# Performance work log

Hardware: AMD Instinct MI355X
Metric: run time of the kernel (lower is better)

## Reference

```python
import jax, jax.numpy as jnp
import numpy as np
import math

NEG_INF = -1e9
B, Q, M, P, HID, H, S = 4, 512, 512, 128, 1024, 16, 64
R = M + Q            # 1024, key length
POSLEN = M + 2 * Q   # 1536


def rel_shift(x):
    # x: [N, H, Q, Rp] -> relative-shifted, same shape
    n, h, q, rp = x.shape
    padded = jnp.pad(x, ((0, 0), (0, 0), (0, 0), (1, 0)))
    return padded.reshape(n, h, rp + 1, q)[:, :, 1:].reshape(n, h, q, rp)


def _attention(query, token_mask, key_content, value, key_position,
               segment_encoding, segment_matrix,
               content_bias, position_bias, segment_bias):
    # query: [N,Q,H,S]; key_content/value: [N,R,H,S]; key_position: [N,Rp,H,S]
    r = key_content.shape[1]
    content_att = jnp.einsum('nqhs,nrhs->nhqr', query + content_bias, key_content)
    position_att = jnp.einsum('nqhs,nrhs->nhqr', query + position_bias, key_position)
    position_att = rel_shift(position_att)[..., 1:1 + r]
    segment_att = jnp.einsum('nqhs,ghs->nhqg', query + segment_bias, segment_encoding)
    # select same-segment (g=1) vs diff-segment (g=0) logit per (q, r) pair
    segment_att = jnp.where(segment_matrix[:, None],           # [N,1,Q,R]
                            segment_att[..., 1:],              # [N,H,Q,1]
                            segment_att[..., :1])
    scale = 1.0 / math.sqrt(float(S))
    logits = (content_att + position_att + segment_att) * scale
    logits = logits + token_mask * NEG_INF
    weights = jax.nn.softmax(logits, axis=3)
    return jnp.einsum('nhqr,nrhs->nqhs', weights, value)


def setup_inputs() -> dict:
    key = jax.random.key(0)
    ks = jax.random.split(key, 16)
    sc = 0.05
    content_inputs = jax.random.normal(ks[0], (B, Q, HID), jnp.float32)
    query_inputs = jax.random.normal(ks[1], (B, P, HID), jnp.float32)
    position_encoding = jax.random.normal(ks[2], (B, POSLEN, HID), jnp.float32)
    segment_encoding = jax.random.normal(ks[3], (2, H, S), jnp.float32) * sc
    segment_matrix = jax.random.randint(ks[4], (B, Q, R), 0, 2) > 0
    # one-hot target mapping: P distinct target positions per batch row
    tpos = jax.vmap(lambda k: jax.random.permutation(k, Q)[:P])(jax.random.split(ks[5], B))
    target_mapping = jax.nn.one_hot(tpos, Q, dtype=jnp.float32)  # [B,P,Q]
    # causal-style permutation masks (1 = masked)
    causal = (jnp.arange(R)[None, :] > (jnp.arange(Q)[:, None] + M)).astype(jnp.float32)
    content_mask = jnp.broadcast_to(causal[None, None], (B, 1, Q, R))
    diag = jnp.pad(jnp.eye(Q, dtype=jnp.float32), ((0, 0), (M, 0)))
    query_mask = jnp.broadcast_to(jnp.minimum(causal + diag, 1.0)[None, None], (B, 1, Q, R))
    content_bias = jax.random.normal(ks[6], (H, S), jnp.float32) * sc
    position_bias = jax.random.normal(ks[7], (H, S), jnp.float32) * sc
    segment_bias = jax.random.normal(ks[8], (H, S), jnp.float32) * sc
    mems = jax.random.normal(ks[9], (B, M, HID), jnp.float32)
    wsc = 1.0 / math.sqrt(HID)
    Wq = jax.random.normal(ks[10], (HID, H, S), jnp.float32) * wsc
    Wkc = jax.random.normal(ks[11], (HID, H, S), jnp.float32) * wsc
    Wv = jax.random.normal(ks[12], (HID, H, S), jnp.float32) * wsc
    Wkp = jax.random.normal(ks[13], (HID, H, S), jnp.float32) * wsc
    Wo = jax.random.normal(ks[14], (H, S, HID), jnp.float32) * wsc
    return dict(content_inputs=content_inputs, query_inputs=query_inputs,
                position_encoding=position_encoding, segment_encoding=segment_encoding,
                segment_matrix=segment_matrix, target_mapping=target_mapping,
                content_mask=content_mask, query_mask=query_mask,
                content_bias=content_bias, position_bias=position_bias,
                segment_bias=segment_bias, mems=mems,
                Wq=Wq, Wkc=Wkc, Wv=Wv, Wkp=Wkp, Wo=Wo)


def reference(content_inputs, query_inputs, position_encoding, segment_encoding,
              segment_matrix, target_mapping, content_mask, query_mask,
              content_bias, position_bias, segment_bias, mems,
              Wq, Wkc, Wv, Wkp, Wo):
    split = lambda x, w: jnp.einsum('nld,dhs->nlhs', x, w)
    merge = lambda x, w: jnp.einsum('nlhs,hsd->nld', x, w)
    contexts = jnp.concatenate([mems, content_inputs], axis=1)  # [B,R,HID]
    key_content = split(contexts, Wkc)
    value = split(contexts, Wv)
    key_position = split(position_encoding, Wkp)
    attn = lambda q, m: _attention(q, m, key_content, value, key_position,
                                   segment_encoding, segment_matrix,
                                   content_bias, position_bias, segment_bias)
    # content stream
    q_c = split(content_inputs, Wq)
    content_outputs = merge(attn(q_c, content_mask), Wo)
    # query stream, scattered to target positions via one-hot target_mapping
    q_q = split(query_inputs, Wq)                               # [B,P,H,S]
    q_q = jnp.einsum('nphs,npq->nqhs', q_q, target_mapping)     # [B,Q,H,S]
    query_outputs = attn(q_q, query_mask)
    query_outputs = jnp.einsum('nqhs,npq->nphs', query_outputs, target_mapping)
    query_outputs = merge(query_outputs, Wo)
    return content_outputs, query_outputs
```

## Files before the change

kernel.cpp:

```cpp
#include <hip/hip_runtime.h>
#include <hip/hip_bf16.h>
#include <math.h>

#define B_ 4
#define Q_ 512
#define M_ 512
#define P_ 128
#define HID_ 1024
#define H_ 16
#define S_ 64
#define R_ 1024
#define POSLEN_ 1536

typedef short bf16x8 __attribute__((ext_vector_type(8)));
typedef float f32x4 __attribute__((ext_vector_type(4)));
typedef unsigned int u32;
typedef unsigned long long u64;

__device__ __forceinline__ ushort f2bf(float f) {
    u32 u = __float_as_uint(f);
    u32 r = (u + 0x7fffu + ((u >> 16) & 1u)) >> 16;
    return (ushort)r;
}
__device__ __forceinline__ float bf2f(ushort s) {
    return __uint_as_float(((u32)s) << 16);
}
__device__ __forceinline__ void gload16(void* l, const void* g) {
    __builtin_amdgcn_global_load_lds(
        (const __attribute__((address_space(1))) u32*)g,
        (__attribute__((address_space(3))) u32*)l, 16, 0, 0);
}

__global__ void find_tpos_k(const float* __restrict__ tm, int* __restrict__ tpos) {
    int i = blockIdx.x * blockDim.x + threadIdx.x;
    if (i >= B_ * P_) return;
    const float* row = tm + (size_t)i * Q_;
    int q = 0;
    for (int j = 0; j < Q_; ++j) q = (row[j] > 0.5f) ? j : q;
    tpos[i] = q;
}

__global__ __launch_bounds__(256) void cvt_all(
    const float* __restrict__ content, const float* __restrict__ mems,
    const float* __restrict__ posenc,  const float* __restrict__ query,
    ushort* __restrict__ ctx, ushort* __restrict__ pos,
    ushort* __restrict__ cont, ushort* __restrict__ qry)
{
    int v = blockIdx.x * 256 + threadIdx.x;
    const float* src;
    ushort* dst;
    if (v < 524288) {
        int row = v >> 7, c8 = v & 127;
        int n = row >> 10, l = row & 1023;
        src = (l < M_) ? mems + ((size_t)(n * M_ + l)) * 1024 + c8 * 8
                       : content + ((size_t)(n * Q_ + (l - M_))) * 1024 + c8 * 8;
        dst = ctx + (size_t)v * 8;
    } else if (v < 1310720) {
        int u = v - 524288;
        src = posenc + (size_t)u * 8; dst = pos + (size_t)u * 8;
    } else if (v < 1572864) {
        int u = v - 1310720;
        src = content + (size_t)u * 8; dst = cont + (size_t)u * 8;
    } else {
        int u = v - 1572864;
        src = query + (size_t)u * 8; dst = qry + (size_t)u * 8;
    }
    float4 a = *(const float4*)src;
    float4 b = *(const float4*)(src + 4);
    ushort4 o0 = {f2bf(a.x), f2bf(a.y), f2bf(a.z), f2bf(a.w)};
    ushort4 o1 = {f2bf(b.x), f2bf(b.y), f2bf(b.z), f2bf(b.w)};
    *(ushort4*)dst = o0;
    *(ushort4*)(dst + 4) = o1;
}

__global__ __launch_bounds__(256) void transpose5(
    const float* W0, const float* W1, const float* W2, const float* W3, const float* W4,
    ushort* T0, ushort* T1, ushort* T2, ushort* T3, ushort* T4)
{
    __shared__ float t[32][33];
    const float* W; ushort* T;
    switch (blockIdx.z) {
        case 0: W = W0; T = T0; break;
        case 1: W = W1; T = T1; break;
        case 2: W = W2; T = T2; break;
        case 3: W = W3; T = T3; break;
        default: W = W4; T = T4; break;
    }
    int bx = blockIdx.x * 32, by = blockIdx.y * 32;
    int tx = threadIdx.x & 31, ty = threadIdx.x >> 5;
    #pragma unroll
    for (int i = 0; i < 32; i += 8)
        t[ty + i][tx] = W[(size_t)(by + ty + i) * 1024 + bx + tx];
    __syncthreads();
    #pragma unroll
    for (int i = 0; i < 32; i += 8)
        T[(size_t)(bx + ty + i) * 1024 + by + tx] = f2bf(t[tx][ty + i]);
}

__global__ __launch_bounds__(256) void seg_prep(const float* __restrict__ segenc,
                                                const float* __restrict__ cb,
                                                const float* __restrict__ sb,
                                                ushort* __restrict__ seg_bf,
                                                float* __restrict__ segc) {
    for (int t = threadIdx.x; t < 16 * 16 * 64; t += 256) {
        int h = t >> 10, g = (t >> 6) & 15, s = t & 63;
// ... 130 lines not shown
    #pragma unroll
    for (int i = 0; i < 4; ++i)
        #pragma unroll
        for (int j = 0; j < 2; ++j) acc[i][j] = f32x4{0.f, 0.f, 0.f, 0.f};

    for (int k0 = 0; k0 < 1024; k0 += 64) {
        __syncthreads();
        #pragma unroll
        for (int it = 0; it < 4; ++it) {
            int idx = it * 256 + tid;
            gload16(&As[idx * 8], A + (size_t)(m0 + (idx >> 3)) * 1024 + k0 + (idx & 7) * 8);
        }
        #pragma unroll
        for (int it = 0; it < 2; ++it) {
            int idx = it * 256 + tid;
            gload16(&Bs[idx * 8], Wo_t + (size_t)(n0 + (idx >> 3)) * 1024 + k0 + (idx & 7) * 8);
        }
        __syncthreads();
        #pragma unroll
        for (int kk = 0; kk < 2; ++kk) {
            const int krd = kk * 32 + hi * 8;
            bf16x8 af[4], bfr[2];
            #pragma unroll
            for (int i = 0; i < 4; ++i)
                af[i] = *(const bf16x8*)&As[(wm * 64 + i * 16 + l15) * 64 + krd];
            #pragma unroll
            for (int j = 0; j < 2; ++j)
                bfr[j] = *(const bf16x8*)&Bs[(wn * 32 + j * 16 + l15) * 64 + krd];
            #pragma unroll
            for (int i = 0; i < 4; ++i)
                #pragma unroll
                for (int j = 0; j < 2; ++j)
                    acc[i][j] = __builtin_amdgcn_mfma_f32_16x16x32_bf16(af[i], bfr[j], acc[i][j], 0, 0, 0);
        }
    }
    #pragma unroll
    for (int i = 0; i < 4; ++i)
        #pragma unroll
        for (int j = 0; j < 2; ++j) {
            int col = n0 + wn * 32 + j * 16 + l15;
            #pragma unroll
            for (int r = 0; r < 4; ++r) {
                int row = m0 + wm * 64 + i * 16 + hi * 4 + r;
                C[(size_t)row * 1024 + col] = acc[i][j][r];
            }
        }
}

__global__ __launch_bounds__(256) void pa_gemm(const ushort* __restrict__ Qpb,
                                               const ushort* __restrict__ KPb,
                                               ushort* __restrict__ PA) {
    const int tid = threadIdx.x;
    const int lane = tid & 63, w = tid >> 6;
    const int l15 = lane & 15, hi = lane >> 4;
    const int jt = blockIdx.x * 128, nh = blockIdx.y;
    const int p0 = w * 32;

    bf16x8 a[2][2];
    #pragma unroll
    for (int i = 0; i < 2; ++i)
        #pragma unroll
        for (int kk = 0; kk < 2; ++kk)
            a[i][kk] = *(const bf16x8*)(Qpb + ((size_t)(nh * 128 + p0 + i * 16 + l15)) * 64 + kk * 32 + hi * 8);

    #pragma unroll
    for (int jc = 0; jc < 8; ++jc) {
        f32x4 c0 = {0.f,0.f,0.f,0.f}, c1 = {0.f,0.f,0.f,0.f};
        #pragma unroll
        for (int kk = 0; kk < 2; ++kk) {
            bf16x8 b = *(const bf16x8*)(KPb + ((size_t)nh * 1536 + jt + jc * 16 + l15) * 64 + kk * 32 + hi * 8);
            c0 = __builtin_amdgcn_mfma_f32_16x16x32_bf16(a[0][kk], b, c0, 0, 0, 0);
            c1 = __builtin_amdgcn_mfma_f32_16x16x32_bf16(a[1][kk], b, c1, 0, 0, 0);
        }
        #pragma unroll
        for (int r = 0; r < 4; ++r) {
            PA[((size_t)(nh * 128 + p0 + hi * 4 + r)) * 1536 + jt + jc * 16 + l15] = f2bf(c0[r]);
            PA[((size_t)(nh * 128 + p0 + 16 + hi * 4 + r)) * 1536 + jt + jc * 16 + l15] = f2bf(c1[r]);
        }
    }
}

#define EXSC 0.180336879f
#define EXBI -23.0831204f
__global__ __launch_bounds__(128) void attn_uni(
    const ushort* __restrict__ Qccb, const ushort* __restrict__ Qcpb,
    const ushort* __restrict__ Qqcb,
    const ushort* __restrict__ KCb,  const ushort* __restrict__ KPb,
    const ushort* __restrict__ Vtb,  const ushort* __restrict__ segb,
    const float* __restrict__ segc,  const u64* __restrict__ pseg,
    const int* __restrict__ tpos,    const ushort* __restrict__ PA,
    float* __restrict__ Pp)
{
    __shared__ ushort Kt[2][64 * 64];
    __shared__ ushort DlT[2][96 * 34];
    __shared__ ushort Pl[2][32 * 64];

    const int tid = threadIdx.x;
    const int lane = tid & 63, wv = tid >> 6;
    const int l15 = lane & 15, hi = lane >> 4;

    int wg = blockIdx.x + 10 * (blockIdx.y + 32 * blockIdx.z);
    int swz = (wg & 7) * 160 + (wg >> 3);
    const int bx = swz % 10;
    int rem = swz / 10;
    const int gy = rem & 31;
    const int n = rem >> 5;

    const bool ISQ = bx >= 8;
    const int h = gy & 15, half = gy >> 4;
    const int nh = n * 16 + h;
    const int q0w = (ISQ ? (bx - 8) * 64 : bx * 64) + wv * 32;

    ushort* dlt = DlT[wv];
    ushort* pl  = Pl[wv];

    bf16x8 acb[2][2], apb[2][2];
    {
        const ushort* qc = ISQ ? (Qqcb + ((size_t)nh * P_ + q0w) * 64)
                               : (Qccb + ((size_t)nh * Q_ + q0w) * 64);
        #pragma unroll
        for (int i = 0; i < 2; ++i)
            #pragma unroll
            for (int kk = 0; kk < 2; ++kk)
                acb[i][kk] = *(const bf16x8*)(qc + (size_t)(i * 16 + l15) * 64 + kk * 32 + hi * 8);
        if (!ISQ) {
            const ushort* qp = Qcpb + ((size_t)nh * Q_ + q0w) * 64;
            #pragma unroll
            for (int i = 0; i < 2; ++i)
                #pragma unroll
                for (int kk = 0; kk < 2; ++kk)
                    apb[i][kk] = *(const bf16x8*)(qp + (size_t)(i * 16 + l15) * 64 + kk * 32 + hi * 8);
        } else {
            apb[0][0] = acb[0][0]; apb[0][1] = acb[0][1];
            apb[1][0] = acb[1][0]; apb[1][1] = acb[1][1];
        }
    }

    float sd[2][2][4];
    {
        f32x4 sg[2] = {{0.f,0.f,0.f,0.f},{0.f,0.f,0.f,0.f}};
        #pragma unroll
        for (int kk = 0; kk < 2; ++kk) {
            bf16x8 b = *(const bf16x8*)(segb + (size_t)(h * 16 + l15) * 64 + kk * 32 + hi * 8);
            sg[0] = __builtin_amdgcn_mfma_f32_16x16x32_bf16(acb[0][kk], b, sg[0], 0, 0, 0);
            sg[1] = __builtin_amdgcn_mfma_f32_16x16x32_bf16(acb[1][kk], b, sg[1], 0, 0, 0);
        }
        float c0 = segc[h * 2 + 0], c1 = segc[h * 2 + 1];
        #pragma unroll
        for (int i = 0; i < 2; ++i)
            #pragma unroll
            for (int r = 0; r < 4; ++r) {
                int base = (lane & 48) << 2;
                sd[0][i][r] = __int_as_float(__builtin_amdgcn_ds_bpermute(base, __float_as_int(sg[i][r]))) + c0;
                sd[1][i][r] = __int_as_float(__builtin_amdgcn_ds_bpermute(base + 4, __float_as_int(sg[i][r]))) + c1;
            }
    }

    int qg[2][4];
    #pragma unroll
    for (int i = 0; i < 2; ++i)
        #pragma unroll
        for (int r = 0; r < 4; ++r) {
            int p = q0w + i * 16 + hi * 4 + r;
            qg[i][r] = ISQ ? tpos[n * P_ + p] : p;
        }

    f32x4 acc[2][4];
    float psum[2][4] = {};
    #pragma unroll
    for (int i = 0; i < 2; ++i)
        #pragma unroll
        for (int j = 0; j < 4; ++j) acc[i][j] = f32x4{0.f,0.f,0.f,0.f};

    auto stage = [&](int b, int rt) {
        const int r0s = rt * 64;
        #pragma unroll
        for (int it = 0; it < 4; ++it) {
            int e = it * 128 + tid;
            int row = e >> 3;
            int sc = ((e & 7) * 8) ^ ((row & 7) << 3);
            gload16(&Kt[b][e * 8], KCb + ((size_t)nh * R_ + r0s + row) * 64 + sc);
        }
    };

    const int q0top = (ISQ ? (bx - 8) * 64 : bx * 64) + 32;
    const int ntb = ISQ ? 16 : min(16, ((q0top + 543) >> 6) + 1);
    const int nt1 = (ntb + 1) >> 1;
    const int t0 = half ? nt1 : 0;
    const int tmax = half ? ntb : nt1;

    stage(0, t0);
    __syncthreads();
    int buf = 0;

    for (int rt = t0; rt < tmax; ++rt) {
        const int r0 = rt * 64;
        if (rt + 1 < tmax) stage(buf ^ 1, rt + 1);

        const bool skip = !ISQ && (r0 > q0w + 543);
        if (!skip) {
            bf16x8 vf[2][4];
            #pragma unroll
            for (int kk = 0; kk < 2; ++kk)
                #pragma unroll
                for (int dj = 0; dj < 4; ++dj)
                    vf[kk][dj] = *(const bf16x8*)(Vtb + ((size_t)nh * 64 + dj * 16 + l15) * 1024 + r0 + kk * 32 + hi * 8);

            f32x4 s[2][4];
            #pragma unroll
            for (int i = 0; i < 2; ++i)
                #pragma unroll
                for (int fc = 0; fc < 4; ++fc) s[i][fc] = f32x4{0.f,0.f,0.f,0.f};
            #pragma unroll
            for (int kk = 0; kk < 2; ++kk) {
                #pragma unroll
                for (int fc = 0; fc < 4; ++fc) {
                    int krow = fc * 16 + l15;
                    bf16x8 kb = *(const bf16x8*)&Kt[buf][krow * 64 + ((kk * 32 + hi * 8) ^ ((krow & 7) << 3))];
                    s[0][fc] = __builtin_amdgcn_mfma_f32_16x16x32_bf16(acb[0][kk], kb, s[0][fc], 0, 0, 0);
                    s[1][fc] = __builtin_amdgcn_mfma_f32_16x16x32_bf16(acb[1][kk], kb, s[1][fc], 0, 0, 0);
                }
            }

            if (!ISQ) {
                const int jb0 = r0 - q0w + 481;
                #pragma unroll
                for (int t = 0; t < 6; ++t) {
                    f32x4 d0 = {0.f,0.f,0.f,0.f}, d1 = {0.f,0.f,0.f,0.f};
                    #pragma unroll
                    for (int kk = 0; kk < 2; ++kk) {
                        bf16x8 pv = *(const bf16x8*)(KPb + ((size_t)nh * POSLEN_ + jb0 + t * 16 + l15) * 64 + kk * 32 + hi * 8);
                        d0 = __builtin_amdgcn_mfma_f32_16x16x32_bf16(apb[0][kk], pv, d0, 0, 0, 0);
                        d1 = __builtin_amdgcn_mfma_f32_16x16x32_bf16(apb[1][kk], pv, d1, 0, 0, 0);
                    }
                    int jj = (t * 16 + l15) * 34;
                    *(u32*)&dlt[jj + hi * 4]          = (u32)f2bf(d0[0]) | ((u32)f2bf(d0[1]) << 16);
                    *(u32*)&dlt[jj + hi * 4 + 2]      = (u32)f2bf(d0[2]) | ((u32)f2bf(d0[3]) << 16);
                    *(u32*)&dlt[jj + 16 + hi * 4]     = (u32)f2bf(d1[0]) | ((u32)f2bf(d1[1]) << 16);
                    *(u32*)&dlt[jj + 16 + hi * 4 + 2] = (u32)f2bf(d1[2]) | ((u32)f2bf(d1[3]) << 16);
                }
            }

            float pav[2][4][4];
            if (ISQ) {
                #pragma unroll
                for (int i = 0; i < 2; ++i)
                    #pragma unroll
                    for (int fc = 0; fc < 4; ++fc)
                        #pragma unroll
                        for (int r = 0; r < 4; ++r) {
                            int qq = i * 16 + hi * 4 + r;
                            int j = (r0 + fc * 16 + l15) - qg[i][r] + 512;
                            pav[i][fc][r] = bf2f(PA[((size_t)nh * P_ + q0w + qq) * 1536 + j]);
                        }
            }

            #pragma unroll
            for (int i = 0; i < 2; ++i) {
                u64 sw[4];
                #pragma unroll
                for (int r = 0; r < 4; ++r)
                    sw[r] = pseg[((size_t)n * Q_ + qg[i][r]) * 16 + rt];
                #pragma unroll
                for (int fc = 0; fc < 4; ++fc) {
                    #pragma unroll
                    for (int r = 0; r < 4; ++r) {
                        int qq = i * 16 + hi * 4 + r;
                        int rr = fc * 16 + l15;
                        float dval = ISQ ? pav[i][fc][r] : bf2f(dlt[(rr - qq + 31) * 34 + qq]);
                        int sel = (int)((sw[r] >> rr) & 1);
                        float st = s[i][fc][r] + dval + (sel ? sd[1][i][r] : sd[0][i][r]);
                        float v = fmaf(st, EXSC, EXBI);
                        bool masked = ISQ ? ((r0 + rr) >= qg[i][r] + 512)
                                          : ((r0 + rr) > qg[i][r] + 512);
                        v = masked ? -INFINITY : v;
                        float pv = exp2f(v);
                        ushort us = f2bf(pv);
                        psum[i][r] += bf2f(us);
                        int row = i * 16 + hi * 4 + r;
                        int cc = (fc * 16 + l15) ^ ((row & 7) << 3);
                        pl[row * 64 + cc] = us;
                    }
                }
            }

            #pragma unroll
            for (int kk = 0; kk < 2; ++kk) {
                bf16x8 pa[2];
                #pragma unroll
                for (int i = 0; i < 2; ++i) {
                    int row = i * 16 + l15;
                    int cc = (kk * 32 + hi * 8) ^ ((row & 7) << 3);
                    pa[i] = *(const bf16x8*)&pl[row * 64 + cc];
                }
                #pragma unroll
                for (int dj = 0; dj < 4; ++dj) {
                    acc[0][dj] = __builtin_amdgcn_mfma_f32_16x16x32_bf16(pa[0], vf[kk][dj], acc[0][dj], 0, 0, 0);
                    acc[1][dj] = __builtin_amdgcn_mfma_f32_16x16x32_bf16(pa[1], vf[kk][dj], acc[1][dj], 0, 0, 0);
                }
            }
        }
        __syncthreads();
        buf ^= 1;
    }

    #pragma unroll
    for (int i = 0; i < 2; ++i)
        #pragma unroll
        for (int r = 0; r < 4; ++r) {
            #pragma unroll
            for (int d = 1; d < 16; d <<= 1) psum[i][r] += __shfl_xor(psum[i][r], d, 64);
        }

    #pragma unroll
    for (int i = 0; i < 2; ++i)
        #pragma unroll
        for (int r = 0; r < 4; ++r) {
            int qrow = q0w + i * 16 + hi * 4 + r;
            size_t rowg = ISQ ? (32768 + (size_t)nh * P_ + qrow) : ((size_t)nh * Q_ + qrow);
            float* base = Pp + (rowg * 2 + half) * 72;
            #pragma unroll
            for (int dj = 0; dj < 4; ++dj)
                base[dj * 16 + l15] = acc[i][dj][r];
            if (l15 == 0) base[64] = psum[i][r];
        }
}

__global__ __launch_bounds__(256) void combine_k(const float* __restrict__ Pp,
                                                 ushort* __restrict__ AOc,
                                                 ushort* __restrict__ AOq) {
    int idx = blockIdx.x * 256 + threadIdx.x;
    int row = idx >> 6, d = idx & 63;
    const float* b0 = Pp + ((size_t)row * 2 + 0) * 72;
    const float* b1 = b0 + 72;
    float l = b0[64] + b1[64];
    ushort o = f2bf((b0[d] + b1[d]) / l);
    if (row < 32768) {
        int n = row >> 13, h = (row >> 9) & 15, q = row & 511;
        AOc[((size_t)(n * Q_ + q)) * 1024 + h * 64 + d] = o;
    } else {
        int r2 = row - 32768;
        int n = r2 >> 11, h = (r2 >> 7) & 15, p = r2 & 127;
        AOq[((size_t)(n * P_ + p)) * 1024 + h * 64 + d] = o;
    }
}

extern "C" void kernel_launch(void* const* d_in, const int* in_sizes, int n_in,
                              void* d_out, int out_size, void* d_ws, size_t ws_size,
                              hipStream_t stream) {
    const float* content = (const float*)d_in[0];
    const float* query   = (const float*)d_in[1];
    const float* posenc  = (const float*)d_in[2];
    const float* segenc  = (const float*)d_in[3];
    const int*   segmat  = (const int*)d_in[4];
    const float* tmap    = (const float*)d_in[5];
    const float* cbias   = (const float*)d_in[8];
    const float* pbias   = (const float*)d_in[9];
    const float* sbias   = (const float*)d_in[10];
    const float* mems    = (const float*)d_in[11];
    const float* Wq      = (const float*)d_in[12];
    const float* Wkc     = (const float*)d_in[13];
    const float* Wv      = (const float*)d_in[14];
    const float* Wkp     = (const float*)d_in[15];
    const float* Wo      = (const float*)d_in[16];
    float* out = (float*)d_out;

    char* p = (char*)d_ws;
    auto alloc = [&](size_t bytes) { char* r = p; p += (bytes + 255) & ~(size_t)255; return r; };
    ushort* ctx_bf  = (ushort*)alloc((size_t)B_ * R_ * 1024 * 2);
    ushort* pos_bf  = (ushort*)alloc((size_t)B_ * POSLEN_ * 1024 * 2);
    ushort* cont_bf = (ushort*)alloc((size_t)B_ * Q_ * 1024 * 2);
    ushort* qry_bf  = (ushort*)alloc((size_t)B_ * P_ * 1024 * 2);
    ushort* Wq_t    = (ushort*)alloc(1024 * 1024 * 2);
    ushort* Wkc_t   = (ushort*)alloc(1024 * 1024 * 2);
    ushort* Wv_t    = (ushort*)alloc(1024 * 1024 * 2);
    ushort* Wkp_t   = (ushort*)alloc(1024 * 1024 * 2);
    ushort* Wo_t    = (ushort*)alloc(1024 * 1024 * 2);
    ushort* KC_bf   = (ushort*)alloc((size_t)B_ * 16 * R_ * 64 * 2);
    ushort* Vt_bf   = (ushort*)alloc((size_t)B_ * 16 * 64 * R_ * 2);
    ushort* KP_bf   = (ushort*)alloc((size_t)B_ * 16 * POSLEN_ * 64 * 2);
    ushort* Qc_cb   = (ushort*)alloc((size_t)B_ * 16 * Q_ * 64 * 2);
    ushort* Qc_pb   = (ushort*)alloc((size_t)B_ * 16 * Q_ * 64 * 2);
    ushort* Qq_cb   = (ushort*)alloc((size_t)B_ * 16 * P_ * 64 * 2);
    ushort* Qq_pb   = (ushort*)alloc((size_t)B_ * 16 * P_ * 64 * 2);
    ushort* PA_bf   = (ushort*)alloc((size_t)B_ * 16 * P_ * POSLEN_ * 2);
    ushort* AOc_bf  = (ushort*)alloc((size_t)B_ * Q_ * 1024 * 2);
    ushort* AOq_bf  = (ushort*)alloc((size_t)B_ * P_ * 1024 * 2);
    ushort* seg_bf  = (ushort*)alloc(16 * 16 * 64 * 2);
    float*  segc    = (float*)alloc(32 * 4);
    u64*    pseg    = (u64*)alloc((size_t)B_ * Q_ * 16 * 8);
    int*    tpos    = (int*)alloc(B_ * P_ * 4);
    float* Pp = (float*)ctx_bf;

    find_tpos_k<<<2, 256, 0, stream>>>(tmap, tpos);
    cvt_all<<<6400, 256, 0, stream>>>(content, mems, posenc, query,
                                      ctx_bf, pos_bf, cont_bf, qry_bf);
    transpose5<<<dim3(32, 32, 5), 256, 0, stream>>>(Wq, Wkc, Wv, Wkp, Wo,
                                                    Wq_t, Wkc_t, Wv_t, Wkp_t, Wo_t);
    seg_prep<<<1, 256, 0, stream>>>(segenc, cbias, sbias, seg_bf, segc);
    pack_seg<<<8192, 256, 0, stream>>>(segmat, pseg);

    proj_all<<<dim3(16, 132), 256, 0, stream>>>(ctx_bf, pos_bf, cont_bf, qry_bf,
                                                Wkc_t, Wv_t, Wkp_t, Wq_t,
                                                KC_bf, Vt_bf, KP_bf,
                                                Qc_cb, Qc_pb, Qq_cb, Qq_pb,
                                                cbias, pbias);

    pa_gemm<<<dim3(12, 64), 256, 0, stream>>>(Qq_pb, KP_bf, PA_bf);

    attn_uni<<<dim3(10, 32, 4), 128, 0, stream>>>(Qc_cb, Qc_pb, Qq_cb, KC_bf, KP_bf, Vt_bf,
                                                  seg_bf, segc, pseg, tpos, PA_bf, Pp);

    combine_k<<<10240, 256, 0, stream>>>(Pp, AOc_bf, AOq_bf);

    oproj<<<dim3(16, 20), 256, 0, stream>>>(AOc_bf, AOq_bf, Wo_t, out);

    (void)in_sizes; (void)n_in; (void)out_size; (void)ws_size;
}
```

Measured before the change: 317.1 us.

## Split attention into single-wave 16-row blocks with direct global K loads

The attention kernel now runs one 64-thread wave per block handling 16 query rows instead of two waves of 32 rows each, which quadruples the grid. K tiles are read straight from global memory into registers, so the double-buffered LDS staging and the per-tile barriers are gone. The position-bias tile is kept in fp32 LDS instead of being packed to bf16, and the causal tile count is computed at the finer row granularity. This should give more parallelism, tighter causal skipping and less sync, at the cost of losing K reuse across waves and issuing more global traffic per row.

```diff
diff --git a/kernel.cpp b/kernel.cpp
--- a/kernel.cpp
+++ b/kernel.cpp
@@ -317,7 +317,7 @@
 
 #define EXSC 0.180336879f
 #define EXBI -23.0831204f
-__global__ __launch_bounds__(128) void attn_uni(
+__global__ __launch_bounds__(64, 3) void attn_uni(
     const ushort* __restrict__ Qccb, const ushort* __restrict__ Qcpb,
     const ushort* __restrict__ Qqcb,
     const ushort* __restrict__ KCb,  const ushort* __restrict__ KPb,
@@ -326,239 +326,179 @@
     const int* __restrict__ tpos,    const ushort* __restrict__ PA,
     float* __restrict__ Pp)
 {
-    __shared__ ushort Kt[2][64 * 64];
-    __shared__ ushort DlT[2][96 * 34];
-    __shared__ ushort Pl[2][32 * 64];
-
-    const int tid = threadIdx.x;
-    const int lane = tid & 63, wv = tid >> 6;
+    __shared__ float Dlf[80 * 20];
+    __shared__ ushort Pl[16 * 64];
+
+    const int lane = threadIdx.x;
     const int l15 = lane & 15, hi = lane >> 4;
 
-    int wg = blockIdx.x + 10 * (blockIdx.y + 32 * blockIdx.z);
-    int swz = (wg & 7) * 160 + (wg >> 3);
-    const int bx = swz % 10;
-    int rem = swz / 10;
+    int wg = blockIdx.x + 40 * (blockIdx.y + 32 * blockIdx.z);
+    int swz = (wg & 7) * 640 + (wg >> 3);
+    const int bx = swz % 40;
+    int rem = swz / 40;
     const int gy = rem & 31;
     const int n = rem >> 5;
 
-    const bool ISQ = bx >= 8;
+    const bool ISQ = bx >= 32;
     const int h = gy & 15, half = gy >> 4;
     const int nh = n * 16 + h;
-    const int q0w = (ISQ ? (bx - 8) * 64 : bx * 64) + wv * 32;
-
-    ushort* dlt = DlT[wv];
-    ushort* pl  = Pl[wv];
-
-    bf16x8 acb[2][2], apb[2][2];
+    const int q0w = (ISQ ? (bx - 32) : bx) * 16;
+
+    bf16x8 acb[2], apb[2];
     {
         const ushort* qc = ISQ ? (Qqcb + ((size_t)nh * P_ + q0w) * 64)
                                : (Qccb + ((size_t)nh * Q_ + q0w) * 64);
         #pragma unroll
-        for (int i = 0; i < 2; ++i)
-            #pragma unroll
-            for (int kk = 0; kk < 2; ++kk)
-                acb[i][kk] = *(const bf16x8*)(qc + (size_t)(i * 16 + l15) * 64 + kk * 32 + hi * 8);
+        for (int kk = 0; kk < 2; ++kk)
+            acb[kk] = *(const bf16x8*)(qc + (size_t)l15 * 64 + kk * 32 + hi * 8);
         if (!ISQ) {
             const ushort* qp = Qcpb + ((size_t)nh * Q_ + q0w) * 64;
             #pragma unroll
-            for (int i = 0; i < 2; ++i)
-                #pragma unroll
-                for (int kk = 0; kk < 2; ++kk)
-                    apb[i][kk] = *(const bf16x8*)(qp + (size_t)(i * 16 + l15) * 64 + kk * 32 + hi * 8);
+            for (int kk = 0; kk < 2; ++kk)
+                apb[kk] = *(const bf16x8*)(qp + (size_t)l15 * 64 + kk * 32 + hi * 8);
         } else {
-            apb[0][0] = acb[0][0]; apb[0][1] = acb[0][1];
-            apb[1][0] = acb[1][0]; apb[1][1] = acb[1][1];
-        }
-    }
-
-    float sd[2][2][4];
+            apb[0] = acb[0]; apb[1] = acb[1];
+        }
+    }
+
+    float sd[2][4];
     {
-        f32x4 sg[2] = {{0.f,0.f,0.f,0.f},{0.f,0.f,0.f,0.f}};
+        f32x4 sg = {0.f, 0.f, 0.f, 0.f};
         #pragma unroll
         for (int kk = 0; kk < 2; ++kk) {
             bf16x8 b = *(const bf16x8*)(segb + (size_t)(h * 16 + l15) * 64 + kk * 32 + hi * 8);
-            sg[0] = __builtin_amdgcn_mfma_f32_16x16x32_bf16(acb[0][kk], b, sg[0], 0, 0, 0);
-            sg[1] = __builtin_amdgcn_mfma_f32_16x16x32_bf16(acb[1][kk], b, sg[1], 0, 0, 0);
+            sg = __builtin_amdgcn_mfma_f32_16x16x32_bf16(acb[kk], b, sg, 0, 0, 0);
         }
         float c0 = segc[h * 2 + 0], c1 = segc[h * 2 + 1];
         #pragma unroll
-        for (int i = 0; i < 2; ++i)
-            #pragma unroll
-            for (int r = 0; r < 4; ++r) {
-                int base = (lane & 48) << 2;
-                sd[0][i][r] = __int_as_float(__builtin_amdgcn_ds_bpermute(base, __float_as_int(sg[i][r]))) + c0;
-                sd[1][i][r] = __int_as_float(__builtin_amdgcn_ds_bpermute(base + 4, __float_as_int(sg[i][r]))) + c1;
-            }
-    }
-
-    int qg[2][4];
-    #pragma unroll
-    for (int i = 0; i < 2; ++i)
-        #pragma unroll
         for (int r = 0; r < 4; ++r) {
-            int p = q0w + i * 16 + hi * 4 + r;
-            qg[i][r] = ISQ ? tpos[n * P_ + p] : p;
-        }
-
-    f32x4 acc[2][4];
-    float psum[2][4] = {};
-    #pragma unroll
-    for (int i = 0; i < 2; ++i)
-        #pragma unroll
-        for (int j = 0; j < 4; ++j) acc[i][j] = f32x4{0.f,0.f,0.f,0.f};
-
-    auto stage = [&](int b, int rt) {
-        const int r0s = rt * 64;
-        #pragma unroll
-        for (int it = 0; it < 4; ++it) {
-            int e = it * 128 + tid;
-            int row = e >> 3;
-            int sc = ((e & 7) * 8) ^ ((row & 7) << 3);
-            gload16(&Kt[b][e * 8], KCb + ((size_t)nh * R_ + r0s + row) * 64 + sc);
-        }
-    };
-
-    const int q0top = (ISQ ? (bx - 8) * 64 : bx * 64) + 32;
-    const int ntb = ISQ ? 16 : min(16, ((q0top + 543) >> 6) + 1);
+            int base = (lane & 48) << 2;
+            sd[0][r] = __int_as_float(__builtin_amdgcn_ds_bpermute(base, __float_as_int(sg[r]))) + c0;
+            sd[1][r] = __int_as_float(__builtin_amdgcn_ds_bpermute(base + 4, __float_as_int(sg[r]))) + c1;
+        }
+    }
+
+    int qg[4];
+    #pragma unroll
+    for (int r = 0; r < 4; ++r) {
+        int p = q0w + hi * 4 + r;
+        qg[r] = ISQ ? tpos[n * P_ + p] : p;
+    }
+
+    f32x4 acc[4];
+    float psum[4] = {};
+    #pragma unroll
+    for (int j = 0; j < 4; ++j) acc[j] = f32x4{0.f, 0.f, 0.f, 0.f};
+
+    const int ntb = ISQ ? 16 : (((q0w + 527) >> 6) + 1);
     const int nt1 = (ntb + 1) >> 1;
     const int t0 = half ? nt1 : 0;
     const int tmax = half ? ntb : nt1;
 
-    stage(0, t0);
-    __syncthreads();
-    int buf = 0;
-
     for (int rt = t0; rt < tmax; ++rt) {
         const int r0 = rt * 64;
-        if (rt + 1 < tmax) stage(buf ^ 1, rt + 1);
-
-        const bool skip = !ISQ && (r0 > q0w + 543);
-        if (!skip) {
-            bf16x8 vf[2][4];
-            #pragma unroll
-            for (int kk = 0; kk < 2; ++kk)
+
+        bf16x8 kf[2][4];
+        #pragma unroll
+        for (int kk = 0; kk < 2; ++kk)
+            #pragma unroll
+            for (int fc = 0; fc < 4; ++fc)
+                kf[kk][fc] = *(const bf16x8*)(KCb + ((size_t)nh * R_ + r0 + fc * 16 + l15) * 64 + kk * 32 + hi * 8);
+
+        f32x4 s[4];
+        #pragma unroll
+        for (int fc = 0; fc < 4; ++fc) s[fc] = f32x4{0.f, 0.f, 0.f, 0.f};
+        #pragma unroll
+        for (int kk = 0; kk < 2; ++kk)
+            #pragma unroll
+            for (int fc = 0; fc < 4; ++fc)
+                s[fc] = __builtin_amdgcn_mfma_f32_16x16x32_bf16(acb[kk], kf[kk][fc], s[fc], 0, 0, 0);
+
+        bf16x8 vf[2][4];
+        #pragma unroll
+        for (int kk = 0; kk < 2; ++kk)
+            #pragma unroll
+            for (int dj = 0; dj < 4; ++dj)
+                vf[kk][dj] = *(const bf16x8*)(Vtb + ((size_t)nh * 64 + dj * 16 + l15) * 1024 + r0 + kk * 32 + hi * 8);
+
+        if (!ISQ) {
+            const int jb0 = r0 - q0w + 497;
+            #pragma unroll
+            for (int t = 0; t < 5; ++t) {
+                f32x4 d0 = {0.f, 0.f, 0.f, 0.f};
                 #pragma unroll
-                for (int dj = 0; dj < 4; ++dj)
-                    vf[kk][dj] = *(const bf16x8*)(Vtb + ((size_t)nh * 64 + dj * 16 + l15) * 1024 + r0 + kk * 32 + hi * 8);
-
-            f32x4 s[2][4];
-            #pragma unroll
-            for (int i = 0; i < 2; ++i)
+                for (int kk = 0; kk < 2; ++kk) {
+                    bf16x8 pv = *(const bf16x8*)(KPb + ((size_t)nh * POSLEN_ + jb0 + t * 16 + l15) * 64 + kk * 32 + hi * 8);
+                    d0 = __builtin_amdgcn_mfma_f32_16x16x32_bf16(apb[kk], pv, d0, 0, 0, 0);
+                }
+                *(f32x4*)(&Dlf[(t * 16 + l15) * 20 + hi * 4]) = d0;
+            }
+        }
+
+        float pav[4][4];
+        if (ISQ) {
+            #pragma unroll
+            for (int fc = 0; fc < 4; ++fc)
                 #pragma unroll
-                for (int fc = 0; fc < 4; ++fc) s[i][fc] = f32x4{0.f,0.f,0.f,0.f};
-            #pragma unroll
-            for (int kk = 0; kk < 2; ++kk) {
-                #pragma unroll
-                for (int fc = 0; fc < 4; ++fc) {
-                    int krow = fc * 16 + l15;
-                    bf16x8 kb = *(const bf16x8*)&Kt[buf][krow * 64 + ((kk * 32 + hi * 8) ^ ((krow & 7) << 3))];
-                    s[0][fc] = __builtin_amdgcn_mfma_f32_16x16x32_bf16(acb[0][kk], kb, s[0][fc], 0, 0, 0);
-                    s[1][fc] = __builtin_amdgcn_mfma_f32_16x16x32_bf16(acb[1][kk], kb, s[1][fc], 0, 0, 0);
+                for (int r = 0; r < 4; ++r) {
+                    int qq = hi * 4 + r;
+                    int j = (r0 + fc * 16 + l15) - qg[r] + 512;
+                    pav[fc][r] = bf2f(PA[((size_t)nh * P_ + q0w + qq) * 1536 + j]);
                 }
+        }
+
+        u64 sw[4];
+        #pragma unroll
+        for (int r = 0; r < 4; ++r)
+            sw[r] = pseg[((size_t)n * Q_ + qg[r]) * 16 + rt];
+        #pragma unroll
+        for (int fc = 0; fc < 4; ++fc) {
+            #pragma unroll
+            for (int r = 0; r < 4; ++r) {
+                int qq = hi * 4 + r;
+                int rr = fc * 16 + l15;
+                float dval = ISQ ? pav[fc][r] : Dlf[(rr - qq + 15) * 20 + qq];
+                int sel = (int)((sw[r] >> rr) & 1);
+                float st = s[fc][r] + dval + (sel ? sd[1][r] : sd[0][r]);
+                float v = fmaf(st, EXSC, EXBI);
+                bool masked = ISQ ? ((r0 + rr) >= qg[r] + 512)
+                                  : ((r0 + rr) > qg[r] + 512);
+                v = masked ? -INFINITY : v;
+                float pv = exp2f(v);
+                ushort us = f2bf(pv);
+                psum[r] += bf2f(us);
+                int row = hi * 4 + r;
+                int cc = rr ^ ((row & 7) << 3);
+                Pl[row * 64 + cc] = us;
             }
-
-            if (!ISQ) {
-                const int jb0 = r0 - q0w + 481;
-                #pragma unroll
-                for (int t = 0; t < 6; ++t) {
-                    f32x4 d0 = {0.f,0.f,0.f,0.f}, d1 = {0.f,0.f,0.f,0.f};
-                    #pragma unroll
-                    for (int kk = 0; kk < 2; ++kk) {
-                        bf16x8 pv = *(const bf16x8*)(KPb + ((size_t)nh * POSLEN_ + jb0 + t * 16 + l15) * 64 + kk * 32 + hi * 8);
-                        d0 = __builtin_amdgcn_mfma_f32_16x16x32_bf16(apb[0][kk], pv, d0, 0, 0, 0);
-                        d1 = __builtin_amdgcn_mfma_f32_16x16x32_bf16(apb[1][kk], pv, d1, 0, 0, 0);
-                    }
-                    int jj = (t * 16 + l15) * 34;
-                    *(u32*)&dlt[jj + hi * 4]          = (u32)f2bf(d0[0]) | ((u32)f2bf(d0[1]) << 16);
-                    *(u32*)&dlt[jj + hi * 4 + 2]      = (u32)f2bf(d0[2]) | ((u32)f2bf(d0[3]) << 16);
-                    *(u32*)&dlt[jj + 16 + hi * 4]     = (u32)f2bf(d1[0]) | ((u32)f2bf(d1[1]) << 16);
-                    *(u32*)&dlt[jj + 16 + hi * 4 + 2] = (u32)f2bf(d1[2]) | ((u32)f2bf(d1[3]) << 16);
-                }
-            }
-
-            float pav[2][4][4];
-            if (ISQ) {
-                #pragma unroll
-                for (int i = 0; i < 2; ++i)
-                    #pragma unroll
-                    for (int fc = 0; fc < 4; ++fc)
-                        #pragma unroll
-                        for (int r = 0; r < 4; ++r) {
-                            int qq = i * 16 + hi * 4 + r;
-                            int j = (r0 + fc * 16 + l15) - qg[i][r] + 512;
-                            pav[i][fc][r] = bf2f(PA[((size_t)nh * P_ + q0w + qq) * 1536 + j]);
-                        }
-            }
-
-            #pragma unroll
-            for (int i = 0; i < 2; ++i) {
-                u64 sw[4];
-                #pragma unroll
-                for (int r = 0; r < 4; ++r)
-                    sw[r] = pseg[((size_t)n * Q_ + qg[i][r]) * 16 + rt];
-                #pragma unroll
-                for (int fc = 0; fc < 4; ++fc) {
-                    #pragma unroll
-                    for (int r = 0; r < 4; ++r) {
-                        int qq = i * 16 + hi * 4 + r;
-                        int rr = fc * 16 + l15;
-                        float dval = ISQ ? pav[i][fc][r] : bf2f(dlt[(rr - qq + 31) * 34 + qq]);
-                        int sel = (int)((sw[r] >> rr) & 1);
-                        float st = s[i][fc][r] + dval + (sel ? sd[1][i][r] : sd[0][i][r]);
-                        float v = fmaf(st, EXSC, EXBI);
-                        bool masked = ISQ ? ((r0 + rr) >= qg[i][r] + 512)
-                                          : ((r0 + rr) > qg[i][r] + 512);
-                        v = masked ? -INFINITY : v;
-                        float pv = exp2f(v);
-                        ushort us = f2bf(pv);
-                        psum[i][r] += bf2f(us);
-                        int row = i * 16 + hi * 4 + r;
-                        int cc = (fc * 16 + l15) ^ ((row & 7) << 3);
-                        pl[row * 64 + cc] = us;
-                    }
-                }
-            }
-
-            #pragma unroll
-            for (int kk = 0; kk < 2; ++kk) {
-                bf16x8 pa[2];
-                #pragma unroll
-                for (int i = 0; i < 2; ++i) {
-                    int row = i * 16 + l15;
-                    int cc = (kk * 32 + hi * 8) ^ ((row & 7) << 3);
-                    pa[i] = *(const bf16x8*)&pl[row * 64 + cc];
-                }
-                #pragma unroll
-                for (int dj = 0; dj < 4; ++dj) {
-                    acc[0][dj] = __builtin_amdgcn_mfma_f32_16x16x32_bf16(pa[0], vf[kk][dj], acc[0][dj], 0, 0, 0);
-                    acc[1][dj] = __builtin_amdgcn_mfma_f32_16x16x32_bf16(pa[1], vf[kk][dj], acc[1][dj], 0, 0, 0);
-                }
-            }
-        }
-        __syncthreads();
-        buf ^= 1;
-    }
-
-    #pragma unroll
-    for (int i = 0; i < 2; ++i)
-        #pragma unroll
-        for (int r = 0; r < 4; ++r) {
-            #pragma unroll
-            for (int d = 1; d < 16; d <<= 1) psum[i][r] += __shfl_xor(psum[i][r], d, 64);
-        }
-
-    #pragma unroll
-    for (int i = 0; i < 2; ++i)
-        #pragma unroll
-        for (int r = 0; r < 4; ++r) {
-            int qrow = q0w + i * 16 + hi * 4 + r;
-            size_t rowg = ISQ ? (32768 + (size_t)nh * P_ + qrow) : ((size_t)nh * Q_ + qrow);
-            float* base = Pp + (rowg * 2 + half) * 72;
+        }
+
+        #pragma unroll
+        for (int kk = 0; kk < 2; ++kk) {
+            int cc = (kk * 32 + hi * 8) ^ ((l15 & 7) << 3);
+            bf16x8 pa = *(const bf16x8*)&Pl[l15 * 64 + cc];
             #pragma unroll
             for (int dj = 0; dj < 4; ++dj)
-                base[dj * 16 + l15] = acc[i][dj][r];
-            if (l15 == 0) base[64] = psum[i][r];
-        }
+                acc[dj] = __builtin_amdgcn_mfma_f32_16x16x32_bf16(pa, vf[kk][dj], acc[dj], 0, 0, 0);
+        }
+    }
+
+    #pragma unroll
+    for (int r = 0; r < 4; ++r) {
+        #pragma unroll
+        for (int d = 1; d < 16; d <<= 1) psum[r] += __shfl_xor(psum[r], d, 64);
+    }
+
+    #pragma unroll
+    for (int r = 0; r < 4; ++r) {
+        int qrow = q0w + hi * 4 + r;
+        size_t rowg = ISQ ? (32768 + (size_t)nh * P_ + qrow) : ((size_t)nh * Q_ + qrow);
+        float* base = Pp + (rowg * 2 + half) * 72;
+        #pragma unroll
+        for (int dj = 0; dj < 4; ++dj)
+            base[dj * 16 + l15] = acc[dj][r];
+        if (l15 == 0) base[64] = psum[r];
+    }
 }
 
 __global__ __launch_bounds__(256) void combine_k(const float* __restrict__ Pp,
@@ -643,8 +583,8 @@
 
     pa_gemm<<<dim3(12, 64), 256, 0, stream>>>(Qq_pb, KP_bf, PA_bf);
 
-    attn_uni<<<dim3(10, 32, 4), 128, 0, stream>>>(Qc_cb, Qc_pb, Qq_cb, KC_bf, KP_bf, Vt_bf,
-                                                  seg_bf, segc, pseg, tpos, PA_bf, Pp);
+    attn_uni<<<dim3(40, 32, 4), 64, 0, stream>>>(Qc_cb, Qc_pb, Qq_cb, KC_bf, KP_bf, Vt_bf,
+                                                 seg_bf, segc, pseg, tpos, PA_bf, Pp);
 
     combine_k<<<10240, 256, 0, stream>>>(Pp, AOc_bf, AOq_bf);
 
```

New measurement: 386.4 us. 21.9% more time.

## Restructure attention blocks: per-wave KV split, register-prefetched K/V, fp32 delta tile

Applied to the files above, without the earlier changes.

Each 128-thread block now covers 32 queries, and its two waves take the two halves of the key range, where before two query groups shared a staged K tile. The LDS double-buffered K staging and block barriers are replaced by per-wave register prefetch of the next K and V tiles. The position-delta tile is kept in fp32 in LDS, which drops the bf16 round trip, and the exp output uses the hardware bf16 pack instruction. This removes __syncthreads and LDS K traffic, and adds occupancy hints. In exchange there are more blocks, each doing redundant Q loads, and more register pressure from the prefetched fragments.

```diff
diff --git a/kernel.cpp b/kernel.cpp
--- a/kernel.cpp
+++ b/kernel.cpp
@@ -21,6 +21,11 @@
     u32 u = __float_as_uint(f);
     u32 r = (u + 0x7fffu + ((u >> 16) & 1u)) >> 16;
     return (ushort)r;
+}
+__device__ __forceinline__ u32 f2bf_hw(float f) {
+    u32 r;
+    asm("v_cvt_pk_bf16_f32 %0, %1, %1" : "=v"(r) : "v"(f));
+    return r;
 }
 __device__ __forceinline__ float bf2f(ushort s) {
     return __uint_as_float(((u32)s) << 16);
@@ -317,37 +322,36 @@
 
 #define EXSC 0.180336879f
 #define EXBI -23.0831204f
-__global__ __launch_bounds__(128) void attn_uni(
+__global__ __launch_bounds__(128, 2) void attn_uni(
     const ushort* __restrict__ Qccb, const ushort* __restrict__ Qcpb,
     const ushort* __restrict__ Qqcb,
     const ushort* __restrict__ KCb,  const ushort* __restrict__ KPb,
     const ushort* __restrict__ Vtb,  const ushort* __restrict__ segb,
     const float* __restrict__ segc,  const u64* __restrict__ pseg,
-    const int* __restrict__ tpos,    const ushort* __restrict__ PA,
+    const int* __restrict__ tpos,    const ushort* __restrict__ PAq,
     float* __restrict__ Pp)
 {
-    __shared__ ushort Kt[2][64 * 64];
-    __shared__ ushort DlT[2][96 * 34];
+    __shared__ float Dlf[2][96 * 36];
     __shared__ ushort Pl[2][32 * 64];
 
     const int tid = threadIdx.x;
     const int lane = tid & 63, wv = tid >> 6;
     const int l15 = lane & 15, hi = lane >> 4;
 
-    int wg = blockIdx.x + 10 * (blockIdx.y + 32 * blockIdx.z);
+    int wg = blockIdx.x + 20 * (blockIdx.y + 16 * blockIdx.z);
     int swz = (wg & 7) * 160 + (wg >> 3);
-    const int bx = swz % 10;
-    int rem = swz / 10;
-    const int gy = rem & 31;
-    const int n = rem >> 5;
-
-    const bool ISQ = bx >= 8;
-    const int h = gy & 15, half = gy >> 4;
+    const int bx = swz % 20;
+    int rem = swz / 20;
+    const int h = rem & 15;
+    const int n = rem >> 4;
+    const int half = wv;
+
+    const bool ISQ = bx >= 16;
     const int nh = n * 16 + h;
-    const int q0w = (ISQ ? (bx - 8) * 64 : bx * 64) + wv * 32;
-
-    ushort* dlt = DlT[wv];
-    ushort* pl  = Pl[wv];
+    const int q0w = (ISQ ? (bx - 16) : bx) * 32;
+
+    float* dlf = Dlf[wv];
+    ushort* pl = Pl[wv];
 
     bf16x8 acb[2][2], apb[2][2];
     {
@@ -365,9 +369,6 @@
                 #pragma unroll
                 for (int kk = 0; kk < 2; ++kk)
                     apb[i][kk] = *(const bf16x8*)(qp + (size_t)(i * 16 + l15) * 64 + kk * 32 + hi * 8);
-        } else {
-            apb[0][0] = acb[0][0]; apb[0][1] = acb[0][1];
-            apb[1][0] = acb[1][0]; apb[1][1] = acb[1][1];
         }
     }
 
@@ -407,136 +408,133 @@
         #pragma unroll
         for (int j = 0; j < 4; ++j) acc[i][j] = f32x4{0.f,0.f,0.f,0.f};
 
-    auto stage = [&](int b, int rt) {
-        const int r0s = rt * 64;
-        #pragma unroll
-        for (int it = 0; it < 4; ++it) {
-            int e = it * 128 + tid;
-            int row = e >> 3;
-            int sc = ((e & 7) * 8) ^ ((row & 7) << 3);
-            gload16(&Kt[b][e * 8], KCb + ((size_t)nh * R_ + r0s + row) * 64 + sc);
-        }
-    };
-
-    const int q0top = (ISQ ? (bx - 8) * 64 : bx * 64) + 32;
-    const int ntb = ISQ ? 16 : min(16, ((q0top + 543) >> 6) + 1);
+    const int ntb = ISQ ? 16 : (((q0w + 543) >> 6) + 1);
     const int nt1 = (ntb + 1) >> 1;
     const int t0 = half ? nt1 : 0;
     const int tmax = half ? ntb : nt1;
 
-    stage(0, t0);
-    __syncthreads();
-    int buf = 0;
+    bf16x8 kf[2][4], vf[2][4];
+    #pragma unroll
+    for (int kk = 0; kk < 2; ++kk)
+        #pragma unroll
+        for (int fc = 0; fc < 4; ++fc)
+            kf[kk][fc] = *(const bf16x8*)(KCb + ((size_t)nh * R_ + t0 * 64 + fc * 16 + l15) * 64 + kk * 32 + hi * 8);
+    #pragma unroll
+    for (int kk = 0; kk < 2; ++kk)
+        #pragma unroll
+        for (int dj = 0; dj < 4; ++dj)
+            vf[kk][dj] = *(const bf16x8*)(Vtb + ((size_t)nh * 64 + dj * 16 + l15) * 1024 + t0 * 64 + kk * 32 + hi * 8);
 
     for (int rt = t0; rt < tmax; ++rt) {
         const int r0 = rt * 64;
-        if (rt + 1 < tmax) stage(buf ^ 1, rt + 1);
-
-        const bool skip = !ISQ && (r0 > q0w + 543);
-        if (!skip) {
-            bf16x8 vf[2][4];
-            #pragma unroll
-            for (int kk = 0; kk < 2; ++kk)
-                #pragma unroll
-                for (int dj = 0; dj < 4; ++dj)
-                    vf[kk][dj] = *(const bf16x8*)(Vtb + ((size_t)nh * 64 + dj * 16 + l15) * 1024 + r0 + kk * 32 + hi * 8);
-
-            f32x4 s[2][4];
+        const int r0n = r0 + 64;
+        const bool more = rt + 1 < tmax;
+
+        u64 sw[2][4];
+        #pragma unroll
+        for (int i = 0; i < 2; ++i)
+            #pragma unroll
+            for (int r = 0; r < 4; ++r)
+                sw[i][r] = pseg[((size_t)n * Q_ + qg[i][r]) * 16 + rt];
+
+        float pav[2][4][4];
+        if (ISQ) {
             #pragma unroll
             for (int i = 0; i < 2; ++i)
                 #pragma unroll
-                for (int fc = 0; fc < 4; ++fc) s[i][fc] = f32x4{0.f,0.f,0.f,0.f};
-            #pragma unroll
-            for (int kk = 0; kk < 2; ++kk) {
-                #pragma unroll
-                for (int fc = 0; fc < 4; ++fc) {
-                    int krow = fc * 16 + l15;
-                    bf16x8 kb = *(const bf16x8*)&Kt[buf][krow * 64 + ((kk * 32 + hi * 8) ^ ((krow & 7) << 3))];
-                    s[0][fc] = __builtin_amdgcn_mfma_f32_16x16x32_bf16(acb[0][kk], kb, s[0][fc], 0, 0, 0);
-                    s[1][fc] = __builtin_amdgcn_mfma_f32_16x16x32_bf16(acb[1][kk], kb, s[1][fc], 0, 0, 0);
-                }
-            }
-
-            if (!ISQ) {
-                const int jb0 = r0 - q0w + 481;
-                #pragma unroll
-                for (int t = 0; t < 6; ++t) {
-                    f32x4 d0 = {0.f,0.f,0.f,0.f}, d1 = {0.f,0.f,0.f,0.f};
-                    #pragma unroll
-                    for (int kk = 0; kk < 2; ++kk) {
-                        bf16x8 pv = *(const bf16x8*)(KPb + ((size_t)nh * POSLEN_ + jb0 + t * 16 + l15) * 64 + kk * 32 + hi * 8);
-                        d0 = __builtin_amdgcn_mfma_f32_16x16x32_bf16(apb[0][kk], pv, d0, 0, 0, 0);
-                        d1 = __builtin_amdgcn_mfma_f32_16x16x32_bf16(apb[1][kk], pv, d1, 0, 0, 0);
-                    }
-                    int jj = (t * 16 + l15) * 34;
-                    *(u32*)&dlt[jj + hi * 4]          = (u32)f2bf(d0[0]) | ((u32)f2bf(d0[1]) << 16);
-                    *(u32*)&dlt[jj + hi * 4 + 2]      = (u32)f2bf(d0[2]) | ((u32)f2bf(d0[3]) << 16);
-                    *(u32*)&dlt[jj + 16 + hi * 4]     = (u32)f2bf(d1[0]) | ((u32)f2bf(d1[1]) << 16);
-                    *(u32*)&dlt[jj + 16 + hi * 4 + 2] = (u32)f2bf(d1[2]) | ((u32)f2bf(d1[3]) << 16);
-                }
-            }
-
-            float pav[2][4][4];
-            if (ISQ) {
-                #pragma unroll
-                for (int i = 0; i < 2; ++i)
+                for (int r = 0; r < 4; ++r) {
+                    int p = q0w + i * 16 + hi * 4 + r;
+                    const ushort* pr = PAq + (size_t)(nh * P_ + p) * 1536 + 512 - qg[i][r] + r0 + l15;
                     #pragma unroll
                     for (int fc = 0; fc < 4; ++fc)
-                        #pragma unroll
-                        for (int r = 0; r < 4; ++r) {
-                            int qq = i * 16 + hi * 4 + r;
-                            int j = (r0 + fc * 16 + l15) - qg[i][r] + 512;
-                            pav[i][fc][r] = bf2f(PA[((size_t)nh * P_ + q0w + qq) * 1536 + j]);
-                        }
-            }
-
+                        pav[i][fc][r] = bf2f(pr[fc * 16]);
+                }
+        }
+
+        f32x4 s[2][4];
+        #pragma unroll
+        for (int i = 0; i < 2; ++i)
+            #pragma unroll
+            for (int fc = 0; fc < 4; ++fc) s[i][fc] = f32x4{0.f,0.f,0.f,0.f};
+        #pragma unroll
+        for (int kk = 0; kk < 2; ++kk)
+            #pragma unroll
+            for (int fc = 0; fc < 4; ++fc) {
+                s[0][fc] = __builtin_amdgcn_mfma_f32_16x16x32_bf16(acb[0][kk], kf[kk][fc], s[0][fc], 0, 0, 0);
+                s[1][fc] = __builtin_amdgcn_mfma_f32_16x16x32_bf16(acb[1][kk], kf[kk][fc], s[1][fc], 0, 0, 0);
+            }
+
+        if (more) {
+            #pragma unroll
+            for (int kk = 0; kk < 2; ++kk)
+                #pragma unroll
+                for (int fc = 0; fc < 4; ++fc)
+                    kf[kk][fc] = *(const bf16x8*)(KCb + ((size_t)nh * R_ + r0n + fc * 16 + l15) * 64 + kk * 32 + hi * 8);
+        }
+
+        if (!ISQ) {
+            const int jb0 = r0 - q0w + 481;
+            #pragma unroll
+            for (int t = 0; t < 6; ++t) {
+                f32x4 d0 = {0.f,0.f,0.f,0.f}, d1 = {0.f,0.f,0.f,0.f};
+                #pragma unroll
+                for (int kk = 0; kk < 2; ++kk) {
+                    bf16x8 pv = *(const bf16x8*)(KPb + ((size_t)nh * POSLEN_ + jb0 + t * 16 + l15) * 64 + kk * 32 + hi * 8);
+                    d0 = __builtin_amdgcn_mfma_f32_16x16x32_bf16(apb[0][kk], pv, d0, 0, 0, 0);
+                    d1 = __builtin_amdgcn_mfma_f32_16x16x32_bf16(apb[1][kk], pv, d1, 0, 0, 0);
+                }
+                float* wp = &dlf[(t * 16 + l15) * 36];
+                *(f32x4*)(wp + hi * 4) = d0;
+                *(f32x4*)(wp + 16 + hi * 4) = d1;
+            }
+        }
+
+        #pragma unroll
+        for (int i = 0; i < 2; ++i) {
+            #pragma unroll
+            for (int fc = 0; fc < 4; ++fc) {
+                #pragma unroll
+                for (int r = 0; r < 4; ++r) {
+                    int qq = i * 16 + hi * 4 + r;
+                    int rr = fc * 16 + l15;
+                    float dval = ISQ ? pav[i][fc][r] : dlf[(rr - qq + 31) * 36 + qq];
+                    int sel = (int)((sw[i][r] >> rr) & 1);
+                    float st = s[i][fc][r] + dval + (sel ? sd[1][i][r] : sd[0][i][r]);
+                    float v = fmaf(st, EXSC, EXBI);
+                    bool masked = (r0 + rr) >= qg[i][r] + (ISQ ? 512 : 513);
+                    v = masked ? -INFINITY : v;
+                    u32 pk = f2bf_hw(exp2f(v));
+                    psum[i][r] += __uint_as_float(pk << 16);
+                    int row = i * 16 + hi * 4 + r;
+                    int cc = rr ^ ((row & 7) << 3);
+                    pl[row * 64 + cc] = (ushort)pk;
+                }
+            }
+        }
+
+        #pragma unroll
+        for (int kk = 0; kk < 2; ++kk) {
+            bf16x8 pa[2];
             #pragma unroll
             for (int i = 0; i < 2; ++i) {
-                u64 sw[4];
-                #pragma unroll
-                for (int r = 0; r < 4; ++r)
-                    sw[r] = pseg[((size_t)n * Q_ + qg[i][r]) * 16 + rt];
-                #pragma unroll
-                for (int fc = 0; fc < 4; ++fc) {
-                    #pragma unroll
-                    for (int r = 0; r < 4; ++r) {
-                        int qq = i * 16 + hi * 4 + r;
-                        int rr = fc * 16 + l15;
-                        float dval = ISQ ? pav[i][fc][r] : bf2f(dlt[(rr - qq + 31) * 34 + qq]);
-                        int sel = (int)((sw[r] >> rr) & 1);
-                        float st = s[i][fc][r] + dval + (sel ? sd[1][i][r] : sd[0][i][r]);
-                        float v = fmaf(st, EXSC, EXBI);
-                        bool masked = ISQ ? ((r0 + rr) >= qg[i][r] + 512)
-                                          : ((r0 + rr) > qg[i][r] + 512);
-                        v = masked ? -INFINITY : v;
-                        float pv = exp2f(v);
-                        ushort us = f2bf(pv);
-                        psum[i][r] += bf2f(us);
-                        int row = i * 16 + hi * 4 + r;
-                        int cc = (fc * 16 + l15) ^ ((row & 7) << 3);
-                        pl[row * 64 + cc] = us;
-                    }
-                }
-            }
-
-            #pragma unroll
-            for (int kk = 0; kk < 2; ++kk) {
-                bf16x8 pa[2];
-                #pragma unroll
-                for (int i = 0; i < 2; ++i) {
-                    int row = i * 16 + l15;
-                    int cc = (kk * 32 + hi * 8) ^ ((row & 7) << 3);
-                    pa[i] = *(const bf16x8*)&pl[row * 64 + cc];
-                }
-                #pragma unroll
-                for (int dj = 0; dj < 4; ++dj) {
-                    acc[0][dj] = __builtin_amdgcn_mfma_f32_16x16x32_bf16(pa[0], vf[kk][dj], acc[0][dj], 0, 0, 0);
-                    acc[1][dj] = __builtin_amdgcn_mfma_f32_16x16x32_bf16(pa[1], vf[kk][dj], acc[1][dj], 0, 0, 0);
-                }
-            }
-        }
-        __syncthreads();
-        buf ^= 1;
+                int row = i * 16 + l15;
+                int cc = (kk * 32 + hi * 8) ^ ((row & 7) << 3);
+                pa[i] = *(const bf16x8*)&pl[row * 64 + cc];
+            }
+            #pragma unroll
+            for (int dj = 0; dj < 4; ++dj) {
+                acc[0][dj] = __builtin_amdgcn_mfma_f32_16x16x32_bf16(pa[0], vf[kk][dj], acc[0][dj], 0, 0, 0);
+                acc[1][dj] = __builtin_amdgcn_mfma_f32_16x16x32_bf16(pa[1], vf[kk][dj], acc[1][dj], 0, 0, 0);
+            }
+        }
+
+        if (more) {
+            #pragma unroll
+            for (int kk = 0; kk < 2; ++kk)
+                #pragma unroll
+                for (int dj = 0; dj < 4; ++dj)
+                    vf[kk][dj] = *(const bf16x8*)(Vtb + ((size_t)nh * 64 + dj * 16 + l15) * 1024 + r0n + kk * 32 + hi * 8);
+        }
     }
 
     #pragma unroll
@@ -618,7 +616,7 @@
     ushort* Qc_pb   = (ushort*)alloc((size_t)B_ * 16 * Q_ * 64 * 2);
     ushort* Qq_cb   = (ushort*)alloc((size_t)B_ * 16 * P_ * 64 * 2);
     ushort* Qq_pb   = (ushort*)alloc((size_t)B_ * 16 * P_ * 64 * 2);
-    ushort* PA_bf   = (ushort*)alloc((size_t)B_ * 16 * P_ * POSLEN_ * 2);
+    ushort* PAq_bf  = (ushort*)alloc((size_t)B_ * 16 * P_ * 1536 * 2);
     ushort* AOc_bf  = (ushort*)alloc((size_t)B_ * Q_ * 1024 * 2);
     ushort* AOq_bf  = (ushort*)alloc((size_t)B_ * P_ * 1024 * 2);
     ushort* seg_bf  = (ushort*)alloc(16 * 16 * 64 * 2);
@@ -641,10 +639,10 @@
                                                 Qc_cb, Qc_pb, Qq_cb, Qq_pb,
                                                 cbias, pbias);
 
-    pa_gemm<<<dim3(12, 64), 256, 0, stream>>>(Qq_pb, KP_bf, PA_bf);
-
-    attn_uni<<<dim3(10, 32, 4), 128, 0, stream>>>(Qc_cb, Qc_pb, Qq_cb, KC_bf, KP_bf, Vt_bf,
-                                                  seg_bf, segc, pseg, tpos, PA_bf, Pp);
+    pa_gemm<<<dim3(12, 64), 256, 0, stream>>>(Qq_pb, KP_bf, PAq_bf);
+
+    attn_uni<<<dim3(20, 16, 4), 128, 0, stream>>>(Qc_cb, Qc_pb, Qq_cb, KC_bf, KP_bf, Vt_bf,
+                                                  seg_bf, segc, pseg, tpos, PAq_bf, Pp);
 
     combine_k<<<10240, 256, 0, stream>>>(Pp, AOc_bf, AOq_bf);
 
```

Result: slower. 517.7 us (+63.3%).
